# Optimization experiments

Hardware: AMD Instinct MI355X
Metric: run time of the kernel (lower is better)

Reference implementation:

```python
import jax, jax.numpy as jnp
import numpy as np

B, HD, NQ, NC, NH, NL, NP, NLAY, DFF = 8, 256, 300, 80, 8, 3, 4, 6, 1024
SHAPES = [(80, 80), (40, 40), (20, 20)]
FEAT_CH = [512, 1024, 2048]
DH = HD // NH
EPS_ANCHOR = 0.01


def _linear(x, w, b):
    return x @ w.T + b


def _ln(x, g, b):
    m = x.mean(-1, keepdims=True)
    v = ((x - m) ** 2).mean(-1, keepdims=True)
    return (x - m) / jnp.sqrt(v + 1e-5) * g + b


def _mlp3(x, w1, b1, w2, b2, w3, b3):
    x = jax.nn.relu(_linear(x, w1, b1))
    x = jax.nn.relu(_linear(x, w2, b2))
    return _linear(x, w3, b3)


def _inv_sigmoid(x, eps=1e-5):
    x = jnp.clip(x, 0.0, 1.0)
    return jnp.log(jnp.clip(x, eps, None) / jnp.clip(1.0 - x, eps, None))


def _anchors():
    parts = []
    for lvl, (h, w) in enumerate(SHAPES):
        gy, gx = jnp.meshgrid(jnp.arange(h, dtype=jnp.float32), jnp.arange(w, dtype=jnp.float32), indexing='ij')
        xy = jnp.stack([(gx + 0.5) / w, (gy + 0.5) / h], -1).reshape(-1, 2)
        wh = jnp.full_like(xy, 0.05 * (2.0 ** lvl))
        parts.append(jnp.concatenate([xy, wh], -1))
    a = jnp.concatenate(parts, 0)[None]  # [1, L, 4]
    valid = jnp.all((a > EPS_ANCHOR) & (a < 1 - EPS_ANCHOR), -1, keepdims=True)
    a = jnp.log(a / (1 - a))
    a = jnp.where(valid, a, jnp.float32(1e6))  # finite sentinel for torch's inf
    return a, valid.astype(jnp.float32)


def _mha(q_in, k_in, v_in, wqkv, bqkv, wo, bo):
    wq, wk, wv = jnp.split(wqkv, 3, 0)
    bq, bk, bv = jnp.split(bqkv, 3, 0)
    q = _linear(q_in, wq, bq)
    k = _linear(k_in, wk, bk)
    v = _linear(v_in, wv, bv)
    Bq = q.shape[0]
    sp = lambda t: t.reshape(Bq, -1, NH, DH).transpose(0, 2, 1, 3)
    q, k, v = sp(q), sp(k), sp(v)
    att = jax.nn.softmax(jnp.einsum('bhqd,bhkd->bhqk', q, k) * (1.0 / np.sqrt(DH)), -1)
    out = jnp.einsum('bhqk,bhkd->bhqd', att, v).transpose(0, 2, 1, 3).reshape(Bq, -1, HD)
    return _linear(out, wo, bo)


def _msda(value, loc, aw):
    # value [B,Len,NH,DH], loc [B,Q,NH,NL,NP,2] in [0,1], aw [B,Q,NH,NL,NP]
    Bq, Q = loc.shape[0], loc.shape[1]
    out = jnp.zeros((Bq, Q, NH, DH), value.dtype)
    start = 0
    for lvl, (h, w) in enumerate(SHAPES):
        v = value[:, start:start + h * w]  # [B,hw,NH,DH]
        start += h * w
        # grid_sample align_corners=False pixel coords
        x = loc[..., lvl, :, 0] * w - 0.5  # [B,Q,NH,NP]
        y = loc[..., lvl, :, 1] * h - 0.5
        x0 = jnp.floor(x)
        y0 = jnp.floor(y)
        lx = x - x0
        ly = y - y0
        acc = jnp.zeros((Bq, Q, NH, NP, DH), value.dtype)
        for dy, dx, wt in ((0, 0, (1 - lx) * (1 - ly)), (0, 1, lx * (1 - ly)), (1, 0, (1 - lx) * ly), (1, 1, lx * ly)):
            xi = x0 + dx
            yi = y0 + dy
            ok = ((xi >= 0) & (xi < w) & (yi >= 0) & (yi < h)).astype(value.dtype)  # zero padding
            idx = (jnp.clip(yi, 0, h - 1) * w + jnp.clip(xi, 0, w - 1)).astype(jnp.int32)
            idxf = idx.transpose(0, 1, 3, 2).reshape(Bq, Q * NP, NH)
            g = jnp.take_along_axis(v, idxf[..., None], axis=1)  # [B,Q*NP,NH,DH]
            g = g.reshape(Bq, Q, NP, NH, DH).transpose(0, 1, 3, 2, 4)
            acc = acc + g * (wt * ok)[..., None]
        out = out + (acc * aw[..., lvl, :, None]).sum(3)
    return out.reshape(Bq, Q, HD)


def reference(feat0, feat1, feat2, pw0, bg0, bb0, pw1, bg1, bb1, pw2, bg2, bb2,
              eo_w, eo_b, eln_g, eln_b, es_w, es_b,
              eb_w1, eb_b1, eb_w2, eb_b2, eb_w3, eb_b3,
              qp_w1, qp_b1, qp_w2, qp_b2,
              d_qkv_w, d_qkv_b, d_ao_w, d_ao_b, d_ln1_g, d_ln1_b,
              d_off_w, d_off_b, d_aw_w, d_aw_b, d_val_w, d_val_b,
              d_out_w, d_out_b, d_ln2_g, d_ln2_b,
              d_f1_w, d_f1_b, d_f2_w, d_f2_b, d_ln3_g, d_ln3_b,
              d_sc_w, d_sc_b, d_bb_w1, d_bb_b1, d_bb_w2, d_bb_b2, d_bb_w3, d_bb_b3):
    feats = [feat0, feat1, feat2]
    pws, bgs, bbs = [pw0, pw1, pw2], [bg0, bg1, bg2], [bb0, bb1, bb2]
    toks = []
    for f, pw, g, b in zip(feats, pws, bgs, bbs):
        # 1x1 conv (no bias) + BatchNorm eval (running mean 0, var 1 -> affine)
        t = jnp.einsum('bchw,oc->bhwo', f, pw) * g + b
        toks.append(t.reshape(f.shape[0], -1, HD))
    memory = jnp.concatenate(toks, 1)  # [B, 8400, 256]
    anchors, valid = _anchors()
    memory = memory * valid
    out_mem = _ln(_linear(memory, eo_w, eo_b), eln_g, eln_b)
    scores = _linear(out_mem, es_w, es_b)  # [B,L,NC]
    _, topi = jax.lax.top_k(scores.max(-1), NQ)  # 'default' query select
    gather = lambda t: jnp.take_along_axis(t, topi[..., None], axis=1)
    sel_mem = gather(out_mem)
    anc_b = jnp.broadcast_to(anchors, (memory.shape[0],) + anchors.shape[1:])
    ref_unact = _mlp3(sel_mem, eb_w1, eb_b1, eb_w2, eb_b2, eb_w3, eb_b3) + gather(anc_b)
    tgt = jax.lax.stop_gradient(sel_mem)
    ref = jax.nn.sigmoid(jax.lax.stop_gradient(ref_unact))  # [B,NQ,4]
    Bq = memory.shape[0]
    for i in range(NLAY):
        qpos = _linear(jax.nn.relu(_linear(ref, qp_w1, qp_b1)), qp_w2, qp_b2)
        q = tgt + qpos
        a = _mha(q, q, tgt, d_qkv_w[i], d_qkv_b[i], d_ao_w[i], d_ao_b[i])
        tgt = _ln(tgt + a, d_ln1_g[i], d_ln1_b[i])
        qc = tgt + qpos
        off = _linear(qc, d_off_w[i], d_off_b[i]).reshape(Bq, NQ, NH, NL, NP, 2)
        aw = jax.nn.softmax(_linear(qc, d_aw_w[i], d_aw_b[i]).reshape(Bq, NQ, NH, NL * NP), -1)
        aw = aw.reshape(Bq, NQ, NH, NL, NP)
        r = ref[:, :, None, None, None, :]
        loc = r[..., :2] + off / NP * r[..., 2:] * 0.5
        val = _linear(memory, d_val_w[i], d_val_b[i]).reshape(Bq, -1, NH, DH)
        ca = _linear(_msda(val, loc, aw), d_out_w[i], d_out_b[i])
        tgt = _ln(tgt + ca, d_ln2_g[i], d_ln2_b[i])
        f = _linear(jax.nn.relu(_linear(tgt, d_f1_w[i], d_f1_b[i])), d_f2_w[i], d_f2_b[i])
        tgt = _ln(tgt + f, d_ln3_g[i], d_ln3_b[i])
        delta = _mlp3(tgt, d_bb_w1[i], d_bb_b1[i], d_bb_w2[i], d_bb_b2[i], d_bb_w3[i], d_bb_b3[i])
        new_ref = jax.nn.sigmoid(delta + _inv_sigmoid(ref))
        ref = jax.lax.stop_gradient(new_ref) if i < NLAY - 1 else new_ref
    logits = _linear(tgt, d_sc_w[-1], d_sc_b[-1])
    return jnp.concatenate([logits, ref], -1)  # [B, NQ, NC+4]


def setup_inputs():
    key = jax.random.key(0)
    ks = iter(jax.random.split(key, 80))
    def rn(shape, s=0.02):
        return jax.random.normal(next(ks), shape, jnp.float32) * s
    inp = {}
    for i, (c, (h, w)) in enumerate(zip(FEAT_CH, SHAPES)):
        inp['feat%d' % i] = rn((B, c, h, w), 1.0)
        inp['pw%d' % i] = rn((HD, c), (2.0 / c) ** 0.5)
        inp['bg%d' % i] = jnp.ones((HD,), jnp.float32)
        inp['bb%d' % i] = jnp.zeros((HD,), jnp.float32)
    inp['eo_w'] = rn((HD, HD)); inp['eo_b'] = jnp.zeros((HD,), jnp.float32)
    inp['eln_g'] = jnp.ones((HD,), jnp.float32); inp['eln_b'] = jnp.zeros((HD,), jnp.float32)
    inp['es_w'] = rn((NC, HD)); inp['es_b'] = jnp.zeros((NC,), jnp.float32)
    inp['eb_w1'] = rn((HD, HD)); inp['eb_b1'] = jnp.zeros((HD,), jnp.float32)
    inp['eb_w2'] = rn((HD, HD)); inp['eb_b2'] = jnp.zeros((HD,), jnp.float32)
    inp['eb_w3'] = rn((4, HD)); inp['eb_b3'] = jnp.zeros((4,), jnp.float32)
    inp['qp_w1'] = rn((2 * HD, 4)); inp['qp_b1'] = jnp.zeros((2 * HD,), jnp.float32)
    inp['qp_w2'] = rn((HD, 2 * HD)); inp['qp_b2'] = jnp.zeros((HD,), jnp.float32)
    L = NLAY
    inp['d_qkv_w'] = rn((L, 3 * HD, HD)); inp['d_qkv_b'] = jnp.zeros((L, 3 * HD), jnp.float32)
    inp['d_ao_w'] = rn((L, HD, HD)); inp['d_ao_b'] = jnp.zeros((L, HD), jnp.float32)
    inp['d_ln1_g'] = jnp.ones((L, HD), jnp.float32); inp['d_ln1_b'] = jnp.zeros((L, HD), jnp.float32)
    inp['d_off_w'] = rn((L, NH * NL * NP * 2, HD), 0.005); inp['d_off_b'] = rn((L, NH * NL * NP * 2), 0.1)
    inp['d_aw_w'] = rn((L, NH * NL * NP, HD)); inp['d_aw_b'] = jnp.zeros((L, NH * NL * NP), jnp.float32)
    inp['d_val_w'] = rn((L, HD, HD)); inp['d_val_b'] = jnp.zeros((L, HD), jnp.float32)
    inp['d_out_w'] = rn((L, HD, HD)); inp['d_out_b'] = jnp.zeros((L, HD), jnp.float32)
    inp['d_ln2_g'] = jnp.ones((L, HD), jnp.float32); inp['d_ln2_b'] = jnp.zeros((L, HD), jnp.float32)
    inp['d_f1_w'] = rn((L, DFF, HD)); inp['d_f1_b'] = jnp.zeros((L, DFF), jnp.float32)
    inp['d_f2_w'] = rn((L, HD, DFF)); inp['d_f2_b'] = jnp.zeros((L, HD), jnp.float32)
    inp['d_ln3_g'] = jnp.ones((L, HD), jnp.float32); inp['d_ln3_b'] = jnp.zeros((L, HD), jnp.float32)
    inp['d_sc_w'] = rn((L, NC, HD)); inp['d_sc_b'] = jnp.zeros((L, NC), jnp.float32)
    inp['d_bb_w1'] = rn((L, HD, HD)); inp['d_bb_b1'] = jnp.zeros((L, HD), jnp.float32)
    inp['d_bb_w2'] = rn((L, HD, HD)); inp['d_bb_b2'] = jnp.zeros((L, HD), jnp.float32)
    inp['d_bb_w3'] = rn((L, 4, HD)); inp['d_bb_b3'] = jnp.zeros((L, 4), jnp.float32)
    return inp
```

## Files before the change

### kernel.cpp

```cpp
#include <hip/hip_runtime.h>

constexpr int Bb  = 8;
constexpr int HDn = 256;
constexpr int NQn = 300;
constexpr int NCn = 80;
constexpr int NHn = 8;
constexpr int NPn = 4;
constexpr int Sn  = 8400;
constexpr int MQ  = Bb * NQn;
constexpr int MS  = Bb * Sn;

typedef __attribute__((ext_vector_type(8))) short short8;
typedef __attribute__((ext_vector_type(4))) float floatx4;

__device__ __forceinline__ unsigned short f2bf(float f) {
    unsigned u = __float_as_uint(f);
    unsigned r = u + 0x7FFFu + ((u >> 16) & 1u);
    return (unsigned short)(r >> 16);
}
__device__ __forceinline__ unsigned pack2(float a, float b) {
    return (unsigned)f2bf(a) | ((unsigned)f2bf(b) << 16);
}

__global__ __launch_bounds__(256) void proj_kernel(
    const float* __restrict__ feat, const float* __restrict__ pw,
    const float* __restrict__ bg, const float* __restrict__ bb,
    float* __restrict__ mem,
    int C, int HW, int Wdim, int base)
{
    const int b = blockIdx.z;
    const float* Afeat = feat + (size_t)b * C * HW;
    __shared__ float As[16][128];
    __shared__ float Ws[16][128];
    const int tid = threadIdx.x;
    const int tx = tid & 15, ty = tid >> 4;
    const int p0 = blockIdx.y * 128, o0 = blockIdx.x * 128;
    const int pp4 = (tid & 31) * 4;
    const int cb = tid >> 5;
    const int wrow = tid >> 1, wk = (tid & 1) * 8;
    float acc[8][8] = {};
    for (int k0 = 0; k0 < C; k0 += 16) {
        float4 va0 = make_float4(0.f, 0.f, 0.f, 0.f), va1 = va0;
        if (p0 + pp4 < HW) {
            va0 = *reinterpret_cast<const float4*>(Afeat + (size_t)(k0 + cb) * HW + p0 + pp4);
            va1 = *reinterpret_cast<const float4*>(Afeat + (size_t)(k0 + cb + 8) * HW + p0 + pp4);
        }
        const float4 w0 = *reinterpret_cast<const float4*>(pw + (size_t)(o0 + wrow) * C + k0 + wk);
        const float4 w1 = *reinterpret_cast<const float4*>(pw + (size_t)(o0 + wrow) * C + k0 + wk + 4);
        __syncthreads();
        As[cb][pp4 + 0] = va0.x; As[cb][pp4 + 1] = va0.y; As[cb][pp4 + 2] = va0.z; As[cb][pp4 + 3] = va0.w;
        As[cb + 8][pp4 + 0] = va1.x; As[cb + 8][pp4 + 1] = va1.y; As[cb + 8][pp4 + 2] = va1.z; As[cb + 8][pp4 + 3] = va1.w;
        Ws[wk + 0][wrow] = w0.x; Ws[wk + 1][wrow] = w0.y; Ws[wk + 2][wrow] = w0.z; Ws[wk + 3][wrow] = w0.w;
        Ws[wk + 4][wrow] = w1.x; Ws[wk + 5][wrow] = w1.y; Ws[wk + 6][wrow] = w1.z; Ws[wk + 7][wrow] = w1.w;
        __syncthreads();
#pragma unroll
        for (int k = 0; k < 16; ++k) {
            const float4 a0 = *reinterpret_cast<const float4*>(&As[k][ty * 8]);
            const float4 a1 = *reinterpret_cast<const float4*>(&As[k][ty * 8 + 4]);
            const float4 wv0 = *reinterpret_cast<const float4*>(&Ws[k][tx * 8]);
            const float4 wv1 = *reinterpret_cast<const float4*>(&Ws[k][tx * 8 + 4]);
            const float av[8] = {a0.x, a0.y, a0.z, a0.w, a1.x, a1.y, a1.z, a1.w};
            const float wv[8] = {wv0.x, wv0.y, wv0.z, wv0.w, wv1.x, wv1.y, wv1.z, wv1.w};
#pragma unroll
            for (int i = 0; i < 8; ++i)
#pragma unroll
                for (int j = 0; j < 8; ++j)
                    acc[i][j] = fmaf(av[i], wv[j], acc[i][j]);
        }
    }
    float bgv[8], bbv[8];
#pragma unroll
    for (int j = 0; j < 8; ++j) { bgv[j] = bg[o0 + tx * 8 + j]; bbv[j] = bb[o0 + tx * 8 + j]; }
#pragma unroll
    for (int i = 0; i < 8; ++i) {
        const int pp = p0 + ty * 8 + i;
        if (pp >= HW) continue;
        const int yy = pp / Wdim, xx = pp - yy * Wdim;
        const float ax = (xx + 0.5f) / Wdim, ay = (yy + 0.5f) / Wdim;
        const float vm = ((ax > 0.01f) && (ax < 0.99f) && (ay > 0.01f) && (ay < 0.99f)) ? 1.f : 0.f;
        float* op = mem + ((size_t)b * Sn + base + pp) * HDn + o0;
#pragma unroll
        for (int j = 0; j < 8; ++j)
            op[tx * 8 + j] = (acc[i][j] * bgv[j] + bbv[j]) * vm;
    }
}

__global__ __launch_bounds__(512) void gemm_eoln(
    const float* __restrict__ A,
    const float* __restrict__ W,
    const float* __restrict__ bias,
    const float* __restrict__ g, const float* __restrict__ bt,
    float* __restrict__ O)
{
    __shared__ float As[16][128];
    __shared__ float Ws[16][256];
    const int tid = threadIdx.x;
    const int tx = tid & 31;
    const int ty = tid >> 5;
    const int m0 = blockIdx.x * 128;
    const int arow = tid >> 2, ak = (tid & 3) * 4;
    const int wrow = tid >> 1, wk = (tid & 1) * 8;
    float acc[8][8] = {};
    for (int k0 = 0; k0 < 256; k0 += 16) {
        const float4 a4 = *reinterpret_cast<const float4*>(A + (size_t)(m0 + arow) * 256 + k0 + ak);
        const float4 w0 = *reinterpret_cast<const float4*>(W + (size_t)wrow * 256 + k0 + wk);
        const float4 w1 = *reinterpret_cast<const float4*>(W + (size_t)wrow * 256 + k0 + wk + 4);
        __syncthreads();
        As[ak + 0][arow] = a4.x; As[ak + 1][arow] = a4.y; As[ak + 2][arow] = a4.z; As[ak + 3][arow] = a4.w;
        Ws[wk + 0][wrow] = w0.x; Ws[wk + 1][wrow] = w0.y; Ws[wk + 2][wrow] = w0.z; Ws[wk + 3][wrow] = w0.w;
        Ws[wk + 4][wrow] = w1.x; Ws[wk + 5][wrow] = w1.y; Ws[wk + 6][wrow] = w1.z; Ws[wk + 7][wrow] = w1.w;
        __syncthreads();
#pragma unroll
        for (int k = 0; k < 16; ++k) {
            const float4 a0 = *reinterpret_cast<const float4*>(&As[k][ty * 8]);
            const float4 a1 = *reinterpret_cast<const float4*>(&As[k][ty * 8 + 4]);
            const float4 wv0 = *reinterpret_cast<const float4*>(&Ws[k][tx * 8]);
            const float4 wv1 = *reinterpret_cast<const float4*>(&Ws[k][tx * 8 + 4]);
            const float av[8] = {a0.x, a0.y, a0.z, a0.w, a1.x, a1.y, a1.z, a1.w};
            const float wv[8] = {wv0.x, wv0.y, wv0.z, wv0.w, wv1.x, wv1.y, wv1.z, wv1.w};
#pragma unroll
            for (int i = 0; i < 8; ++i)
#pragma unroll
                for (int j = 0; j < 8; ++j)
                    acc[i][j] = fmaf(av[i], wv[j], acc[i][j]);
        }
    }
    float bv[8], gv[8], btv[8];
#pragma unroll
    for (int j = 0; j < 8; ++j) {
        bv[j] = bias[tx * 8 + j];
        gv[j] = g[tx * 8 + j];
        btv[j] = bt[tx * 8 + j];
    }
#pragma unroll
    for (int i = 0; i < 8; ++i) {
        float s1 = 0.f, s2 = 0.f;
#pragma unroll
        for (int j = 0; j < 8; ++j) {
            const float v = acc[i][j] + bv[j];
            acc[i][j] = v;
            s1 += v; s2 += v * v;
        }
#pragma unroll
        for (int o = 1; o < 32; o <<= 1) {
            s1 += __shfl_xor(s1, o, 64);
            s2 += __shfl_xor(s2, o, 64);
        }
        const float mean = s1 * (1.f / 256.f);
        const float var  = s2 * (1.f / 256.f) - mean * mean;
        const float inv  = rsqrtf(var + 1e-5f);
        float out[8];
#pragma unroll
        for (int j = 0; j < 8; ++j) out[j] = (acc[i][j] - mean) * inv * gv[j] + btv[j];
        float* op = O + (size_t)(m0 + ty * 8 + i) * 256 + tx * 8;
        *reinterpret_cast<float4*>(op) = make_float4(out[0], out[1], out[2], out[3]);
        *reinterpret_cast<float4*>(op + 4) = make_float4(out[4], out[5], out[6], out[7]);
    }
}

__global__ __launch_bounds__(256) void gemm_es(
    const float* __restrict__ A,
    const float* __restrict__ W,
    const float* __restrict__ bias,
    float* __restrict__ smax)
{
    __shared__ float As[16][128];
    __shared__ float Ws[16][80];
    const int tid = threadIdx.x;
    const int tx = tid & 15;
    const int ty = tid >> 4;
    const int m0 = blockIdx.x * 128;
    const int arow = tid >> 1, ak = (tid & 1) * 8;
    float acc[8][5] = {};
    for (int k0 = 0; k0 < 256; k0 += 16) {
        const float4 a0 = *reinterpret_cast<const float4*>(A + (size_t)(m0 + arow) * 256 + k0 + ak);
        const float4 a1 = *reinterpret_cast<const float4*>(A + (size_t)(m0 + arow) * 256 + k0 + ak + 4);
        float4 w0 = make_float4(0.f,0.f,0.f,0.f), w1 = w0;
        const int wrow = tid >> 1, wk = (tid & 1) * 8;
        if (tid < 160) {
            w0 = *reinterpret_cast<const float4*>(W + (size_t)wrow * 256 + k0 + wk);
            w1 = *reinterpret_cast<const float4*>(W + (size_t)wrow * 256 + k0 + wk + 4);
        }
        __syncthreads();
        As[ak + 0][arow] = a0.x; As[ak + 1][arow] = a0.y; As[ak + 2][arow] = a0.z; As[ak + 3][arow] = a0.w;
        As[ak + 4][arow] = a1.x; As[ak + 5][arow] = a1.y; As[ak + 6][arow] = a1.z; As[ak + 7][arow] = a1.w;
        if (tid < 160) {
            Ws[wk + 0][wrow] = w0.x; Ws[wk + 1][wrow] = w0.y; Ws[wk + 2][wrow] = w0.z; Ws[wk + 3][wrow] = w0.w;
            Ws[wk + 4][wrow] = w1.x; Ws[wk + 5][wrow] = w1.y; Ws[wk + 6][wrow] = w1.z; Ws[wk + 7][wrow] = w1.w;
        }
        __syncthreads();
#pragma unroll
        for (int k = 0; k < 16; ++k) {
            const float4 a4 = *reinterpret_cast<const float4*>(&As[k][ty * 8]);
            const float4 a5 = *reinterpret_cast<const float4*>(&As[k][ty * 8 + 4]);
            const float av[8] = {a4.x, a4.y, a4.z, a4.w, a5.x, a5.y, a5.z, a5.w};
            float wv[5];
#pragma unroll
            for (int j = 0; j < 5; ++j) wv[j] = Ws[k][tx * 5 + j];
#pragma unroll
            for (int i = 0; i < 8; ++i)
#pragma unroll
                for (int j = 0; j < 5; ++j)
                    acc[i][j] = fmaf(av[i], wv[j], acc[i][j]);
        }
    }
    float bv[5];
#pragma unroll
    for (int j = 0; j < 5; ++j) bv[j] = bias[tx * 5 + j];
#pragma unroll
    for (int i = 0; i < 8; ++i) {
        float vmax = -3.0e38f;
#pragma unroll
        for (int j = 0; j < 5; ++j) vmax = fmaxf(vmax, acc[i][j] + bv[j]);
#pragma unroll
        for (int o = 1; o < 16; o <<= 1) vmax = fmaxf(vmax, __shfl_xor(vmax, o, 64));
        if (tx == 0) smax[m0 + ty * 8 + i] = vmax;
    }
}

__global__ void fconv_kernel(const float* __restrict__ in, unsigned short* __restrict__ out, int n4)
{
    const int i = blockIdx.x * 256 + threadIdx.x;
    if (i >= n4) return;
    const float4 v = reinterpret_cast<const float4*>(in)[i];
    reinterpret_cast<uint2*>(out)[i] = make_uint2(pack2(v.x, v.y), pack2(v.z, v.w));
}

__global__ __launch_bounds__(512) void gemm_vbig(
    const unsigned short* __restrict__ A,
    const float* __restrict__ W,
    const float* __restrict__ bias,
    unsigned short* __restrict__ C, int ldc,
    int M)
{
    __shared__ __align__(16) unsigned short As[128 * 40];
    __shared__ __align__(16) unsigned short Bs[256 * 40];
    const int tid = threadIdx.x;
    const int lane = tid & 63, wid = tid >> 6;
    const int wm = wid >> 2, wn = wid & 3;
    const int m0 = blockIdx.x * 128, n0 = blockIdx.y * 256;
    const int arow = tid >> 2, ak = (tid & 3) * 8;
    const int brow = tid >> 1, bk = (tid & 1) * 16;
    const int fs = (lane >> 4) * 8;
    floatx4 acc[4][4];
#pragma unroll
    for (int i = 0; i < 4; ++i)
#pragma unroll
        for (int j = 0; j < 4; ++j) acc[i][j] = (floatx4){0.f, 0.f, 0.f, 0.f};

    for (int k0 = 0; k0 < 256; k0 += 32) {
        const short8 a8 = *reinterpret_cast<const short8*>(A + (size_t)(m0 + arow) * 256 + k0 + ak);
        float wv[16];
        {
            const float* wp = W + (size_t)(n0 + brow) * 256 + k0 + bk;
#pragma unroll
            for (int j = 0; j < 4; ++j) *reinterpret_cast<float4*>(&wv[4 * j]) = *reinterpret_cast<const float4*>(wp + 4 * j);
        }
        __syncthreads();
        *reinterpret_cast<short8*>(&As[arow * 40 + ak]) = a8;
        *reinterpret_cast<uint4*>(&Bs[brow * 40 + bk]) =
            make_uint4(pack2(wv[0], wv[1]), pack2(wv[2], wv[3]), pack2(wv[4], wv[5]), pack2(wv[6], wv[7]));
        *reinterpret_cast<uint4*>(&Bs[brow * 40 + bk + 8]) =
            make_uint4(pack2(wv[8], wv[9]), pack2(wv[10], wv[11]), pack2(wv[12], wv[13]), pack2(wv[14], wv[15]));
        __syncthreads();
        short8 af[4], bf[4];
#pragma unroll
        for (int mi = 0; mi < 4; ++mi)
            af[mi] = *reinterpret_cast<const short8*>(&As[(wm * 64 + mi * 16 + (lane & 15)) * 40 + fs]);
#pragma unroll
        for (int ni = 0; ni < 4; ++ni)
            bf[ni] = *reinterpret_cast<const short8*>(&Bs[(wn * 64 + ni * 16 + (lane & 15)) * 40 + fs]);
#pragma unroll
        for (int mi = 0; mi < 4; ++mi)
#pragma unroll
            for (int ni = 0; ni < 4; ++ni)
                acc[mi][ni] = __builtin_amdgcn_mfma_f32_16x16x32_bf16(af[mi], bf[ni], acc[mi][ni], 0, 0, 0);
    }
#pragma unroll
    for (int mi = 0; mi < 4; ++mi) {
        const int rowb = m0 + wm * 64 + mi * 16 + (lane >> 4) * 4;
#pragma unroll
        for (int ni = 0; ni < 4; ++ni) {
            const int col = n0 + wn * 64 + ni * 16 + (lane & 15);
            const float bv = bias[col];
#pragma unroll
            for (int r = 0; r < 4; ++r)
                C[(size_t)(rowb + r) * ldc + col] = f2bf(acc[mi][ni][r] + bv);
        }
    }
}

template <int ACT>
__global__ __launch_bounds__(256) void gemm_sm(
    const float* __restrict__ A, const float* __restrict__ A2, int a2_nlim, int lda,
    const float* __restrict__ W, int ldw,
    const float* __restrict__ bias,
    float* __restrict__ C, int ldc,
    int M, int N, int K)
{
    constexpr int LD = 264;
    __shared__ __align__(16) unsigned short As[64 * LD];
    __shared__ __align__(16) unsigned short Bs[64 * LD];
    const int tid = threadIdx.x;
    const int lane = tid & 63, wid = tid >> 6;
    const int wr = wid >> 1, wc = wid & 1;
    const int m0 = blockIdx.y * 64, n0 = blockIdx.x * 64;
    const float* A2e = (A2 && n0 < a2_nlim) ? A2 : nullptr;
    const int srow = tid >> 2;
    const int cb   = (tid & 3) * 16;
    const int fs = (lane >> 4) * 8;
    floatx4 acc[2][2];
#pragma unroll
    for (int i = 0; i < 2; ++i)
#pragma unroll
        for (int j = 0; j < 2; ++j) acc[i][j] = (floatx4){0.f, 0.f, 0.f, 0.f};

    for (int kc = 0; kc < K; kc += 256) {
        if (kc) __syncthreads();
        {
            const bool mok = (m0 + srow < M);
            const float* ap = A + (size_t)(m0 + srow) * lda + kc;
            const float* ap2 = A2e ? A2e + (size_t)(m0 + srow) * lda + kc : nullptr;
#pragma unroll
            for (int c = 0; c < 4; ++c) {
                float4 v[4];
#pragma unroll
                for (int j = 0; j < 4; ++j) {
                    v[j] = make_float4(0.f, 0.f, 0.f, 0.f);
                    if (mok) {
                        v[j] = *reinterpret_cast<const float4*>(ap + cb + c * 64 + j * 4);
                        if (ap2) {
                            const float4 v2 = *reinterpret_cast<const float4*>(ap2 + cb + c * 64 + j * 4);
                            v[j].x += v2.x; v[j].y += v2.y; v[j].z += v2.z; v[j].w += v2.w;
                        }
                    }
                }
#pragma unroll
                for (int j = 0; j < 4; ++j)
                    *reinterpret_cast<uint2*>(&As[srow * LD + cb + c * 64 + j * 4]) =
                        make_uint2(pack2(v[j].x, v[j].y), pack2(v[j].z, v[j].w));
            }
        }
        {
            const bool nok = (n0 + srow < N);
            const float* wp = W + (size_t)(n0 + srow) * ldw + kc;
#pragma unroll
            for (int c = 0; c < 4; ++c) {
                float4 v[4];
#pragma unroll
                for (int j = 0; j < 4; ++j) {
                    v[j] = make_float4(0.f, 0.f, 0.f, 0.f);
                    if (nok) v[j] = *reinterpret_cast<const float4*>(wp + cb + c * 64 + j * 4);
                }
#pragma unroll
                for (int j = 0; j < 4; ++j)
                    *reinterpret_cast<uint2*>(&Bs[srow * LD + cb + c * 64 + j * 4]) =
                        make_uint2(pack2(v[j].x, v[j].y), pack2(v[j].z, v[j].w));
            }
        }
        __syncthreads();
#pragma unroll
        for (int ks = 0; ks < 8; ++ks) {
            short8 af[2], bf[2];
#pragma unroll
            for (int mi = 0; mi < 2; ++mi)
                af[mi] = *reinterpret_cast<const short8*>(&As[(wr * 32 + mi * 16 + (lane & 15)) * LD + ks * 32 + fs]);
#pragma unroll
            for (int ni = 0; ni < 2; ++ni)
                bf[ni] = *reinterpret_cast<const short8*>(&Bs[(wc * 32 + ni * 16 + (lane & 15)) * LD + ks * 32 + fs]);
#pragma unroll
            for (int mi = 0; mi < 2; ++mi)
#pragma unroll
                for (int ni = 0; ni < 2; ++ni)
                    acc[mi][ni] = __builtin_amdgcn_mfma_f32_16x16x32_bf16(af[mi], bf[ni], acc[mi][ni], 0, 0, 0);
        }
    }
#pragma unroll
    for (int mi = 0; mi < 2; ++mi) {
        const int rowb = m0 + wr * 32 + mi * 16 + (lane >> 4) * 4;
#pragma unroll
        for (int ni = 0; ni < 2; ++ni) {
            const int col = n0 + wc * 32 + ni * 16 + (lane & 15);
            if (col >= N) continue;
            const float bv = bias[col];
#pragma unroll
            for (int r = 0; r < 4; ++r) {
                const int row = rowb + r;
                if (row >= M) continue;
                float v = acc[mi][ni][r] + bv;
                if (ACT == 1) v = fmaxf(v, 0.f);
                C[(size_t)row * ldc + col] = v;
            }
        }
    }
}

__global__ __launch_bounds__(256) void gemm_qpos(
    const float* __restrict__ ref, const float* __restrict__ w1, const float* __restrict__ b1,
    const float* __restrict__ W2, const float* __restrict__ b2,
    float* __restrict__ C, int M)
{
    __shared__ __align__(16) unsigned short As_h[128 * 40];
    __shared__ __align__(16) unsigned short Bs_h[128 * 40];
    __shared__ float w1s[512 * 4];
    __shared__ float b1s[512];
    const int tid = threadIdx.x;
    const int lane = tid & 63, wid = tid >> 6;
    const int wm = wid >> 1, wn = wid & 1;
    const int m0 = blockIdx.x * 128, n0 = blockIdx.y * 128;
    const int srow = tid >> 1, skoff = (tid & 1) * 16;
    const int fs = (lane >> 4) * 8;
    for (int i = tid; i < 512 * 4; i += 256) w1s[i] = w1[i];
    for (int i = tid; i < 512; i += 256) b1s[i] = b1[i];
    float rv0 = 0.f, rv1 = 0.f, rv2 = 0.f, rv3 = 0.f;
    if (m0 + srow < M) {
        const float* rp = ref + (size_t)(m0 + srow) * 4;
        rv0 = rp[0]; rv1 = rp[1]; rv2 = rp[2]; rv3 = rp[3];
    }
    floatx4 acc[4][4];
#pragma unroll
    for (int i = 0; i < 4; ++i)
#pragma unroll
        for (int j = 0; j < 4; ++j) acc[i][j] = (floatx4){0.f, 0.f, 0.f, 0.f};
    __syncthreads();

    for (int k0 = 0; k0 < 512; k0 += 32) {
        float av[16], wv[16];
#pragma unroll
        for (int j = 0; j < 16; ++j) {
            const int k = k0 + skoff + j;
            const float v = b1s[k] + rv0 * w1s[k * 4] + rv1 * w1s[k * 4 + 1] + rv2 * w1s[k * 4 + 2] + rv3 * w1s[k * 4 + 3];
            av[j] = fmaxf(v, 0.f);
            wv[j] = 0.f;
        }
        if (n0 + srow < 256) {
            const float* wp = W2 + (size_t)(n0 + srow) * 512 + k0 + skoff;
#pragma unroll
            for (int j = 0; j < 4; ++j) *reinterpret_cast<float4*>(&wv[4 * j]) = *reinterpret_cast<const float4*>(wp + 4 * j);
        }
        __syncthreads();
        *reinterpret_cast<uint4*>(&As_h[srow * 40 + skoff]) =
            make_uint4(pack2(av[0], av[1]), pack2(av[2], av[3]), pack2(av[4], av[5]), pack2(av[6], av[7]));
        *reinterpret_cast<uint4*>(&As_h[srow * 40 + skoff + 8]) =
            make_uint4(pack2(av[8], av[9]), pack2(av[10], av[11]), pack2(av[12], av[13]), pack2(av[14], av[15]));
        *reinterpret_cast<uint4*>(&Bs_h[srow * 40 + skoff]) =
            make_uint4(pack2(wv[0], wv[1]), pack2(wv[2], wv[3]), pack2(wv[4], wv[5]), pack2(wv[6], wv[7]));
        *reinterpret_cast<uint4*>(&Bs_h[srow * 40 + skoff + 8]) =
            make_uint4(pack2(wv[8], wv[9]), pack2(wv[10], wv[11]), pack2(wv[12], wv[13]), pack2(wv[14], wv[15]));
        __syncthreads();
        short8 af[4], bff[4];
#pragma unroll
        for (int mi = 0; mi < 4; ++mi) {
            const int r = wm * 64 + mi * 16 + (lane & 15);
            af[mi] = *reinterpret_cast<const short8*>(&As_h[r * 40 + fs]);
        }
#pragma unroll
        for (int ni = 0; ni < 4; ++ni) {
            const int r = wn * 64 + ni * 16 + (lane & 15);
            bff[ni] = *reinterpret_cast<const short8*>(&Bs_h[r * 40 + fs]);
        }
#pragma unroll
        for (int mi = 0; mi < 4; ++mi)
#pragma unroll
            for (int ni = 0; ni < 4; ++ni)
                acc[mi][ni] = __builtin_amdgcn_mfma_f32_16x16x32_bf16(af[mi], bff[ni], acc[mi][ni], 0, 0, 0);
    }
#pragma unroll
    for (int mi = 0; mi < 4; ++mi) {
        const int rowb = m0 + wm * 64 + mi * 16 + (lane >> 4) * 4;
#pragma unroll
        for (int ni = 0; ni < 4; ++ni) {
            const int col = n0 + wn * 64 + ni * 16 + (lane & 15);
            const float bv = b2[col];
#pragma unroll
            for (int r = 0; r < 4; ++r) {
                const int row = rowb + r;
                if (row >= M) continue;
                C[(size_t)row * HDn + col] = acc[mi][ni][r] + bv;
            }
        }
    }
}

__global__ __launch_bounds__(256) void ln_kernel(
    const float* __restrict__ X, const float* __restrict__ R,
    const float* __restrict__ g, const float* __restrict__ bta,
    float* __restrict__ O)
{
    const int m = blockIdx.x;
    const int t = threadIdx.x;
    float v = X[(size_t)m * HDn + t] + R[(size_t)m * HDn + t];
    float s1 = v, s2 = v * v;
#pragma unroll
    for (int o = 32; o > 0; o >>= 1) {
        s1 += __shfl_down(s1, o, 64);
        s2 += __shfl_down(s2, o, 64);
    }
    __shared__ float a1[4], a2[4];
    if ((t & 63) == 0) { a1[t >> 6] = s1; a2[t >> 6] = s2; }
    __syncthreads();
    const float S1 = a1[0] + a1[1] + a1[2] + a1[3];
    const float S2 = a2[0] + a2[1] + a2[2] + a2[3];
    const float mean = S1 * (1.f / HDn);
    const float var  = S2 * (1.f / HDn) - mean * mean;
    const float inv  = rsqrtf(var + 1e-5f);
    O[(size_t)m * HDn + t] = (v - mean) * inv * g[t] + bta[t];
}

__global__ __launch_bounds__(256) void topk_kernel(const float* __restrict__ smax, int* __restrict__ topi)
{
    const int b = blockIdx.x, t = threadIdx.x;
    __shared__ float vals[Sn];
    __shared__ int hist[256];
    __shared__ unsigned long long sel[NQn];
    __shared__ unsigned long long s_prefix;
    __shared__ int s_need;
    __shared__ int s_cnt;
    for (int i = t; i < Sn; i += 256) vals[i] = smax[(size_t)b * Sn + i];
    if (t == 0) { s_prefix = 0ULL; s_need = NQn; s_cnt = 0; }
    __syncthreads();

    for (int shift = 56; shift >= 0; shift -= 8) {
        if (t < 256) hist[t] = 0;
        __syncthreads();
        const unsigned long long prefix = s_prefix;
        const unsigned long long mask = (shift == 56) ? 0ULL : (~0ULL << (shift + 8));
        for (int i = t; i < Sn; i += 256) {
            unsigned uk = __float_as_uint(vals[i]);
            uk = (uk & 0x80000000u) ? ~uk : (uk | 0x80000000u);
            const unsigned long long key = ((unsigned long long)uk << 32) | (unsigned)(Sn - i);
            if ((key & mask) == prefix)
                atomicAdd(&hist[(int)((key >> shift) & 255)], 1);
        }
        __syncthreads();
        if (t == 0) {
            int need = s_need, accum = 0, v = 255;
            for (; v >= 0; --v) {
                const int c = hist[v];
                if (accum + c >= need) break;
                accum += c;
            }
            s_prefix = s_prefix | ((unsigned long long)(unsigned)v << shift);
            s_need = need - accum;
        }
        __syncthreads();
    }
    const unsigned long long thresh = s_prefix;
    for (int i = t; i < Sn; i += 256) {
        unsigned uk = __float_as_uint(vals[i]);
        uk = (uk & 0x80000000u) ? ~uk : (uk | 0x80000000u);
        const unsigned long long key = ((unsigned long long)uk << 32) | (unsigned)(Sn - i);
        if (key >= thresh) {
            const int pos = atomicAdd(&s_cnt, 1);
            if (pos < NQn) sel[pos] = key;
        }
    }
    __syncthreads();
    for (int j = t; j < NQn; j += 256) {
        const unsigned long long kj = sel[j];
        int rank = 0;
        for (int i = 0; i < NQn; ++i) rank += (sel[i] > kj) ? 1 : 0;
        topi[b * NQn + rank] = Sn - (int)(kj & 0xFFFFFFFFULL);
    }
}

__global__ __launch_bounds__(256) void gather_kernel(const float* __restrict__ src, const int* __restrict__ topi,
                                                     float* __restrict__ dst)
{
    const int m = blockIdx.x;
    const int b = m / NQn;
    const int s = topi[m];
    dst[(size_t)m * HDn + threadIdx.x] = src[((size_t)b * Sn + s) * HDn + threadIdx.x];
}

__device__ __forceinline__ void anchor_of(int s, float a[4])
{
    int lvl, p, w;
    if (s < 6400)      { lvl = 0; p = s;        w = 80; }
    else if (s < 8000) { lvl = 1; p = s - 6400; w = 40; }
    else               { lvl = 2; p = s - 8000; w = 20; }
    const int y = p / w, x = p - y * w;
    const float ax = (x + 0.5f) / w, ay = (y + 0.5f) / w;
    const float awh = 0.05f * (float)(1 << lvl);
    const bool valid = (ax > 0.01f) && (ax < 0.99f) && (ay > 0.01f) && (ay < 0.99f);
    if (valid) {
        a[0] = logf(ax / (1.f - ax));
        a[1] = logf(ay / (1.f - ay));
        const float lw = logf(awh / (1.f - awh));
        a[2] = lw; a[3] = lw;
    } else {
        a[0] = a[1] = a[2] = a[3] = 1e6f;
    }
}

template <int MODE>
__global__ __launch_bounds__(256) void head4_kernel(
    const float* __restrict__ A, const float* __restrict__ W, const float* __restrict__ bias,
    const int* __restrict__ topi, float* __restrict__ ref)
{
    const int wv = threadIdx.x >> 6, lane = threadIdx.x & 63;
    const int m = blockIdx.x * 4 + wv;
    if (m >= MQ) return;
    const float4 a = *reinterpret_cast<const float4*>(A + (size_t)m * HDn + lane * 4);
    float d[4];
#pragma unroll
    for (int c = 0; c < 4; ++c) {
        const float4 w = *reinterpret_cast<const float4*>(W + c * HDn + lane * 4);
        float p = a.x * w.x + a.y * w.y + a.z * w.z + a.w * w.w;
#pragma unroll
        for (int o = 32; o > 0; o >>= 1) p += __shfl_xor(p, o, 64);
        d[c] = p;
    }
    if (lane == 0) {
        float base[4];
        if (MODE == 0) {
            anchor_of(topi[m], base);
        } else {
#pragma unroll
            for (int c = 0; c < 4; ++c) {
                float x = ref[m * 4 + c];
                x = fminf(fmaxf(x, 0.f), 1.f);
                base[c] = logf(fmaxf(x, 1e-5f) / fmaxf(1.f - x, 1e-5f));
            }
        }
#pragma unroll
        for (int c = 0; c < 4; ++c) {
            const float x = d[c] + bias[c] + base[c];
            ref[m * 4 + c] = 1.f / (1.f + expf(-x));
        }
    }
}

__global__ __launch_bounds__(320) void mha_kernel(const float* __restrict__ QKV, float* __restrict__ O)
{
    const int h = blockIdx.x, b = blockIdx.y, qs = blockIdx.z;
    __shared__ float Ks[NQn][32];
    __shared__ float Vs[NQn][32];
    __shared__ float Om[152][32];
    __shared__ float Mm[152];
    __shared__ float Lm[152];
    const int t = threadIdx.x;
    for (int i = t; i < NQn * 32; i += 320) {
        const int kk = i >> 5, d = i & 31;
        const size_t src = ((size_t)(b * NQn + kk)) * 768 + h * 32 + d;
        Ks[kk][d] = QKV[src + 256];
        Vs[kk][d] = QKV[src + 512];
    }
    __syncthreads();
    const int half = (t >= 160) ? 1 : 0;
    const int qloc = half ? (t - 160) : t;
    const int q = qs * 150 + qloc;
    float m = -1e30f, l = 0.f;
    float o[32];
    if (qloc < 150) {
        float qv[32];
        const float* qp = QKV + ((size_t)(b * NQn + q)) * 768 + h * 32;
#pragma unroll
        for (int d = 0; d < 32; ++d) qv[d] = qp[d] * 0.17677669529663687f;
#pragma unroll
        for (int d = 0; d < 32; ++d) o[d] = 0.f;
        const int k0 = half * 150, k1 = k0 + 150;
        for (int kk = k0; kk < k1; ++kk) {
            float s0 = 0.f, s1 = 0.f, s2 = 0.f, s3 = 0.f;
#pragma unroll
            for (int d = 0; d < 32; d += 4) {
                s0 = fmaf(qv[d + 0], Ks[kk][d + 0], s0);
                s1 = fmaf(qv[d + 1], Ks[kk][d + 1], s1);
                s2 = fmaf(qv[d + 2], Ks[kk][d + 2], s2);
                s3 = fmaf(qv[d + 3], Ks[kk][d + 3], s3);
            }
            const float s = (s0 + s1) + (s2 + s3);
            if (s > m + 8.f) {
                const float cf = __expf(m - s);
                m = s;
                l *= cf;
#pragma unroll
                for (int d = 0; d < 32; ++d) o[d] *= cf;
            }
            const float pv = __expf(s - m);
            l += pv;
#pragma unroll
            for (int d = 0; d < 32; ++d) o[d] = fmaf(pv, Vs[kk][d], o[d]);
        }
        if (half) {
            Mm[qloc] = m; Lm[qloc] = l;
#pragma unroll
            for (int d = 0; d < 32; ++d) Om[qloc][d] = o[d];
        }
    }
    __syncthreads();
    if (!half && qloc < 150) {
        const float m2 = Mm[qloc], l2 = Lm[qloc];
        const float mm = fmaxf(m, m2);
        const float c1 = __expf(m - mm), c2 = __expf(m2 - mm);
        const float L = l * c1 + l2 * c2;
        const float inv = 1.f / L;
        float* op = O + ((size_t)(b * NQn + q)) * HDn + h * 32;
#pragma unroll
        for (int d = 0; d < 32; ++d) op[d] = (o[d] * c1 + Om[qloc][d] * c2) * inv;
    }
}

__global__ void concat_oaw(const float* __restrict__ offw, const float* __restrict__ offbias,
                           const float* __restrict__ aww, const float* __restrict__ awbias,
                           float* __restrict__ cw, float* __restrict__ cb)
{
    const int idx = blockIdx.x * 256 + threadIdx.x;
    const int TW = 6 * 288 * 256;
    if (idx < TW) {
        const int i = idx / (288 * 256);
        const int r = (idx / 256) % 288;
        const int c = idx & 255;
        cw[idx] = (r < 192) ? offw[((size_t)i * 192 + r) * 256 + c]
                            : aww[((size_t)i * 96 + (r - 192)) * 256 + c];
    } else if (idx < TW + 6 * 288) {
        const int j = idx - TW;
        const int i = j / 288, r = j % 288;
        cb[j] = (r < 192) ? offbias[i * 192 + r] : awbias[i * 96 + (r - 192)];
    }
}

__global__ __launch_bounds__(256) void msda_kernel(const unsigned short* __restrict__ val, int ldv,
                                                   const float* __restrict__ oaw,
                                                   const float* __restrict__ ref,
                                                   float* __restrict__ out)
{
    const int mq = blockIdx.x;
    const int b = mq / NQn;
    const int t = threadIdx.x;
    const int h = t >> 5, d = t & 31;
    __shared__ float s_ref[4];
    __shared__ float s_aw[96];
    __shared__ float s_off[192];
    if (t < 4) s_ref[t] = ref[mq * 4 + t];
    if (t < 96) s_aw[t] = oaw[(size_t)mq * 288 + 192 + t];
    if (t < 192) s_off[t] = oaw[(size_t)mq * 288 + t];
    __syncthreads();
    if (t < 8) {
        float* p = s_aw + t * 12;
        float mx = -1e30f;
#pragma unroll
        for (int i = 0; i < 12; ++i) mx = fmaxf(mx, p[i]);
        float e[12];
        float s = 0.f;
#pragma unroll
        for (int i = 0; i < 12; ++i) { e[i] = expf(p[i] - mx); s += e[i]; }
        const float inv = 1.f / s;
#pragma unroll
        for (int i = 0; i < 12; ++i) p[i] = e[i] * inv;
    }
    __syncthreads();
    const int Wl[3] = {80, 40, 20};
    const int base[3] = {0, 6400, 8000};
    float acc = 0.f;
#pragma unroll
    for (int l = 0; l < 3; ++l) {
        const int W = Wl[l];
        const unsigned short* vb = val + ((size_t)b * Sn + base[l]) * ldv + h * 32 + d;
#pragma unroll
        for (int p = 0; p < 4; ++p) {
            const float ox = s_off[((h * 3 + l) * 4 + p) * 2 + 0];
            const float oy = s_off[((h * 3 + l) * 4 + p) * 2 + 1];
            const float locx = s_ref[0] + ox * (1.f / NPn) * s_ref[2] * 0.5f;
            const float locy = s_ref[1] + oy * (1.f / NPn) * s_ref[3] * 0.5f;
            const float x = locx * W - 0.5f;
            const float y = locy * W - 0.5f;
            const float x0f = floorf(x), y0f = floorf(y);
            const float lx = x - x0f, ly = y - y0f;
            const int x0 = (int)x0f, y0 = (int)y0f;
            const float a = s_aw[h * 12 + l * 4 + p];
            const float wts[4] = {(1.f - lx) * (1.f - ly), lx * (1.f - ly), (1.f - lx) * ly, lx * ly};
            float sum = 0.f;
#pragma unroll
            for (int c2 = 0; c2 < 4; ++c2) {
                const int xi = x0 + (c2 & 1);
                const int yi = y0 + (c2 >> 1);
                const bool ok = (xi >= 0) && (xi < W) && (yi >= 0) && (yi < W);
                const int xc = min(max(xi, 0), W - 1);
                const int yc = min(max(yi, 0), W - 1);
                const float v = __uint_as_float((unsigned)vb[(size_t)(yc * W + xc) * ldv] << 16);
                sum = fmaf(wts[c2], ok ? v : 0.f, sum);
            }
            acc = fmaf(a, sum, acc);
        }
    }
    out[(size_t)mq * HDn + t] = acc;
}

__global__ void copy_ref_kernel(const float* __restrict__ ref, float* __restrict__ out)
{
    const int m = blockIdx.x * 256 + threadIdx.x;
    if (m >= MQ) return;
#pragma unroll
    for (int c = 0; c < 4; ++c) out[(size_t)m * 84 + 80 + c] = ref[m * 4 + c];
}

extern "C" void kernel_launch(void* const* d_in, const int* in_sizes, int n_in,
                              void* d_out, int out_size, void* d_ws, size_t ws_size,
                              hipStream_t stream)
{
    (void)in_sizes; (void)n_in; (void)out_size;
    const float* feat0 = (const float*)d_in[0];
    const float* pw0   = (const float*)d_in[1];
    const float* bg0   = (const float*)d_in[2];
    const float* bb0   = (const float*)d_in[3];
    const float* feat1 = (const float*)d_in[4];
    const float* pw1   = (const float*)d_in[5];
    const float* bg1   = (const float*)d_in[6];
    const float* bb1   = (const float*)d_in[7];
    const float* feat2 = (const float*)d_in[8];
    const float* pw2   = (const float*)d_in[9];
    const float* bg2   = (const float*)d_in[10];
    const float* bb2   = (const float*)d_in[11];
    const float* eo_w  = (const float*)d_in[12];
    const float* eo_b  = (const float*)d_in[13];
    const float* eln_g = (const float*)d_in[14];
    const float* eln_b = (const float*)d_in[15];
    const float* es_w  = (const float*)d_in[16];
    const float* es_b  = (const float*)d_in[17];
    const float* eb_w1 = (const float*)d_in[18];
    const float* eb_b1 = (const float*)d_in[19];
    const float* eb_w2 = (const float*)d_in[20];
    const float* eb_b2 = (const float*)d_in[21];
    const float* eb_w3 = (const float*)d_in[22];
    const float* eb_b3 = (const float*)d_in[23];
    const float* qp_w1 = (const float*)d_in[24];
    const float* qp_b1 = (const float*)d_in[25];
    const float* qp_w2 = (const float*)d_in[26];
    const float* qp_b2 = (const float*)d_in[27];
    const float* d_qkv_w = (const float*)d_in[28];
    const float* d_qkv_b = (const float*)d_in[29];
    const float* d_ao_w  = (const float*)d_in[30];
    const float* d_ao_b  = (const float*)d_in[31];
    const float* d_ln1_g = (const float*)d_in[32];
    const float* d_ln1_b = (const float*)d_in[33];
    const float* d_off_w = (const float*)d_in[34];
    const float* d_off_b = (const float*)d_in[35];
    const float* d_aw_w  = (const float*)d_in[36];
    const float* d_aw_b  = (const float*)d_in[37];
    const float* d_val_w = (const float*)d_in[38];
    const float* d_val_b = (const float*)d_in[39];
    const float* d_out_w = (const float*)d_in[40];
    const float* d_out_b = (const float*)d_in[41];
    const float* d_ln2_g = (const float*)d_in[42];
    const float* d_ln2_b = (const float*)d_in[43];
    const float* d_f1_w  = (const float*)d_in[44];
    const float* d_f1_b  = (const float*)d_in[45];
    const float* d_f2_w  = (const float*)d_in[46];
    const float* d_f2_b  = (const float*)d_in[47];
    const float* d_ln3_g = (const float*)d_in[48];
    const float* d_ln3_b = (const float*)d_in[49];
    const float* d_sc_w  = (const float*)d_in[50];
    const float* d_sc_b  = (const float*)d_in[51];
    const float* d_bb_w1 = (const float*)d_in[52];
    const float* d_bb_b1 = (const float*)d_in[53];
    const float* d_bb_w2 = (const float*)d_in[54];
    const float* d_bb_b2 = (const float*)d_in[55];
    const float* d_bb_w3 = (const float*)d_in[56];
    const float* d_bb_b3 = (const float*)d_in[57];

    float* ws = (float*)d_ws;
    size_t off = 0;
    auto alloc = [&](size_t n) { float* p = ws + off; off += (n + 63) & ~(size_t)63; return p; };
    float* memory = alloc((size_t)MS * HDn);
    float* om     = alloc((size_t)MS * HDn);
    float* smaxb  = alloc((size_t)MS);
    int*   topi   = (int*)alloc((size_t)MQ);
    float* tgt    = alloc((size_t)MQ * HDn);
    float* refb   = alloc((size_t)MQ * 4);
    float* qpos   = alloc((size_t)MQ * HDn);
    float* qkvb   = alloc((size_t)MQ * 768);
    float* atto   = alloc((size_t)MQ * HDn);
    float* abuf   = alloc((size_t)MQ * HDn);
    float* oawb   = alloc((size_t)MQ * 288);
    float* msd    = alloc((size_t)MQ * HDn);
    float* ffb    = alloc((size_t)MQ * 1024);
    float* qb     = alloc((size_t)MQ * HDn);
    float* kb     = alloc((size_t)MQ * HDn);
    float* cw     = alloc((size_t)6 * 288 * 256);
    float* cb     = alloc((size_t)6 * 288);
    const size_t VALBIG_FLOATS = (size_t)MS * 768;
    unsigned short* valbig = nullptr;
    if ((off + VALBIG_FLOATS + 64) * sizeof(float) <= ws_size)
        valbig = (unsigned short*)alloc(VALBIG_FLOATS);
    const bool batched = (valbig != nullptr);
    unsigned short* ombf = (unsigned short*)om;
    float* outp = (float*)d_out;

    concat_oaw<<<(6 * 288 * 256 + 6 * 288 + 255) / 256, 256, 0, stream>>>(d_off_w, d_off_b, d_aw_w, d_aw_b, cw, cb);

    proj_kernel<<<dim3(2, 50, 8), 256, 0, stream>>>(feat0, pw0, bg0, bb0, memory, 512, 6400, 80, 0);
    proj_kernel<<<dim3(2, 13, 8), 256, 0, stream>>>(feat1, pw1, bg1, bb1, memory, 1024, 1600, 40, 6400);
    proj_kernel<<<dim3(2, 4, 8), 256, 0, stream>>>(feat2, pw2, bg2, bb2, memory, 2048, 400, 20, 8000);

    gemm_eoln<<<525, 512, 0, stream>>>(memory, eo_w, eo_b, eln_g, eln_b, om);
    gemm_es<<<525, 256, 0, stream>>>(om, es_w, es_b, smaxb);
    topk_kernel<<<Bb, 256, 0, stream>>>(smaxb, topi);
    gather_kernel<<<MQ, 256, 0, stream>>>(om, topi, tgt);

    gemm_sm<1><<<dim3(4, 38), 256, 0, stream>>>(tgt, nullptr, 0, HDn, eb_w1, HDn, eb_b1, qb, HDn, MQ, HDn, HDn);
    gemm_sm<1><<<dim3(4, 38), 256, 0, stream>>>(qb, nullptr, 0, HDn, eb_w2, HDn, eb_b2, kb, HDn, MQ, HDn, HDn);
    head4_kernel<0><<<600, 256, 0, stream>>>(kb, eb_w3, eb_b3, topi, refb);

    if (batched) {
        fconv_kernel<<<(MS * HDn / 4 + 255) / 256, 256, 0, stream>>>(memory, ombf, MS * HDn / 4);
        gemm_vbig<<<dim3(525, 6), 512, 0, stream>>>(ombf, d_val_w, d_val_b, valbig, 1536, MS);
    }

    for (int i = 0; i < 6; ++i) {
        const float* wqkv = d_qkv_w + (size_t)i * 768 * 256;
        const float* bqkv = d_qkv_b + (size_t)i * 768;
        gemm_qpos<<<dim3(19, 2), 256, 0, stream>>>(refb, qp_w1, qp_b1, qp_w2, qp_b2, qpos, MQ);
        gemm_sm<0><<<dim3(12, 38), 256, 0, stream>>>(tgt, qpos, 512, HDn, wqkv, HDn, bqkv, qkvb, 768, MQ, 768, HDn);
        mha_kernel<<<dim3(NHn, Bb, 2), 320, 0, stream>>>(qkvb, atto);
        gemm_sm<0><<<dim3(4, 38), 256, 0, stream>>>(atto, nullptr, 0, HDn, d_ao_w + (size_t)i * 65536, HDn,
                                                    d_ao_b + (size_t)i * 256, abuf, HDn, MQ, HDn, HDn);
        ln_kernel<<<MQ, 256, 0, stream>>>(abuf, tgt, d_ln1_g + (size_t)i * 256, d_ln1_b + (size_t)i * 256, tgt);
        gemm_sm<0><<<dim3(5, 38), 256, 0, stream>>>(tgt, qpos, 1 << 30, HDn, cw + (size_t)i * 288 * 256, HDn,
                                                    cb + (size_t)i * 288, oawb, 288, MQ, 288, HDn);
        const unsigned short* valptr;
        int ldv;
        if (batched) { valptr = valbig + (size_t)i * 256; ldv = 1536; }
        else {
            fconv_kernel<<<(MS * HDn / 4 + 255) / 256, 256, 0, stream>>>(memory, (unsigned short*)ffb, MS * HDn / 4);
            gemm_vbig<<<dim3(525, 1), 512, 0, stream>>>((unsigned short*)ffb, d_val_w + (size_t)i * 65536,
                                                        d_val_b + (size_t)i * 256, ombf, 256, MS);
            valptr = ombf; ldv = 256;
        }
        msda_kernel<<<MQ, 256, 0, stream>>>(valptr, ldv, oawb, refb, msd);
        gemm_sm<0><<<dim3(4, 38), 256, 0, stream>>>(msd, nullptr, 0, HDn, d_out_w + (size_t)i * 65536, HDn,
                                                    d_out_b + (size_t)i * 256, abuf, HDn, MQ, HDn, HDn);
        ln_kernel<<<MQ, 256, 0, stream>>>(abuf, tgt, d_ln2_g + (size_t)i * 256, d_ln2_b + (size_t)i * 256, tgt);
        gemm_sm<1><<<dim3(16, 38), 256, 0, stream>>>(tgt, nullptr, 0, HDn, d_f1_w + (size_t)i * 1024 * 256, HDn,
                                                     d_f1_b + (size_t)i * 1024, ffb, 1024, MQ, 1024, HDn);
        gemm_sm<0><<<dim3(4, 38), 256, 0, stream>>>(ffb, nullptr, 0, 1024, d_f2_w + (size_t)i * 256 * 1024, 1024,
                                                    d_f2_b + (size_t)i * 256, abuf, HDn, MQ, HDn, 1024);
        ln_kernel<<<MQ, 256, 0, stream>>>(abuf, tgt, d_ln3_g + (size_t)i * 256, d_ln3_b + (size_t)i * 256, tgt);
        gemm_sm<1><<<dim3(4, 38), 256, 0, stream>>>(tgt, nullptr, 0, HDn, d_bb_w1 + (size_t)i * 65536, HDn,
                                                    d_bb_b1 + (size_t)i * 256, qb, HDn, MQ, HDn, HDn);
        gemm_sm<1><<<dim3(4, 38), 256, 0, stream>>>(qb, nullptr, 0, HDn, d_bb_w2 + (size_t)i * 65536, HDn,
                                                    d_bb_b2 + (size_t)i * 256, kb, HDn, MQ, HDn, HDn);
        head4_kernel<1><<<600, 256, 0, stream>>>(kb, d_bb_w3 + (size_t)i * 1024, d_bb_b3 + (size_t)i * 4, nullptr, refb);
    }

    gemm_sm<0><<<dim3(2, 38), 256, 0, stream>>>(tgt, nullptr, 0, HDn, d_sc_w + (size_t)5 * 80 * 256, HDn,
                                                d_sc_b + (size_t)5 * 80, outp, 84, MQ, NCn, HDn);
    copy_ref_kernel<<<(MQ + 255) / 256, 256, 0, stream>>>(refb, outp);
}
```

Measured before the change: 2.543 ms.

## Fuse bf16 memory conversion and ref copy; restripe proj_kernel column mapping

gemm_eoln now writes a bf16 copy of memory while it loads its A tiles, which replaces the separate fconv_kernel pass over the full memory tensor. head4_kernel writes the final reference boxes straight into the output on the last layer, so copy_ref_kernel is gone. proj_kernel switches to a strided column mapping (tx + 16*j) with a scalar LDS read per column instead of float4 reads, and its launch bounds gain a min-blocks hint of 2. These changes remove one memory-sized pass and one launch, but they need extra workspace for the bf16 buffer and may raise register pressure in proj_kernel.

New measurement: 2.662 ms. 4.7% more time.

```diff
diff --git a/kernel.cpp b/kernel.cpp
--- a/kernel.cpp
+++ b/kernel.cpp
@@ -22,7 +22,7 @@
     return (unsigned)f2bf(a) | ((unsigned)f2bf(b) << 16);
 }
 
-__global__ __launch_bounds__(256) void proj_kernel(
+__global__ __launch_bounds__(256, 2) void proj_kernel(
     const float* __restrict__ feat, const float* __restrict__ pw,
     const float* __restrict__ bg, const float* __restrict__ bb,
     float* __restrict__ mem,
@@ -57,10 +57,10 @@
         for (int k = 0; k < 16; ++k) {
             const float4 a0 = *reinterpret_cast<const float4*>(&As[k][ty * 8]);
             const float4 a1 = *reinterpret_cast<const float4*>(&As[k][ty * 8 + 4]);
-            const float4 wv0 = *reinterpret_cast<const float4*>(&Ws[k][tx * 8]);
-            const float4 wv1 = *reinterpret_cast<const float4*>(&Ws[k][tx * 8 + 4]);
             const float av[8] = {a0.x, a0.y, a0.z, a0.w, a1.x, a1.y, a1.z, a1.w};
-            const float wv[8] = {wv0.x, wv0.y, wv0.z, wv0.w, wv1.x, wv1.y, wv1.z, wv1.w};
+            float wv[8];
+#pragma unroll
+            for (int j = 0; j < 8; ++j) wv[j] = Ws[k][tx + 16 * j];
 #pragma unroll
             for (int i = 0; i < 8; ++i)
 #pragma unroll
@@ -70,7 +70,7 @@
     }
     float bgv[8], bbv[8];
 #pragma unroll
-    for (int j = 0; j < 8; ++j) { bgv[j] = bg[o0 + tx * 8 + j]; bbv[j] = bb[o0 + tx * 8 + j]; }
+    for (int j = 0; j < 8; ++j) { bgv[j] = bg[o0 + tx + 16 * j]; bbv[j] = bb[o0 + tx + 16 * j]; }
 #pragma unroll
     for (int i = 0; i < 8; ++i) {
         const int pp = p0 + ty * 8 + i;
@@ -81,7 +81,7 @@
         float* op = mem + ((size_t)b * Sn + base + pp) * HDn + o0;
 #pragma unroll
         for (int j = 0; j < 8; ++j)
-            op[tx * 8 + j] = (acc[i][j] * bgv[j] + bbv[j]) * vm;
+            op[tx + 16 * j] = (acc[i][j] * bgv[j] + bbv[j]) * vm;
     }
 }
 
@@ -90,7 +90,8 @@
     const float* __restrict__ W,
     const float* __restrict__ bias,
     const float* __restrict__ g, const float* __restrict__ bt,
-    float* __restrict__ O)
+    float* __restrict__ O,
+    unsigned short* __restrict__ Abf)
 {
     __shared__ float As[16][128];
     __shared__ float Ws[16][256];
@@ -105,6 +106,9 @@
         const float4 a4 = *reinterpret_cast<const float4*>(A + (size_t)(m0 + arow) * 256 + k0 + ak);
         const float4 w0 = *reinterpret_cast<const float4*>(W + (size_t)wrow * 256 + k0 + wk);
         const float4 w1 = *reinterpret_cast<const float4*>(W + (size_t)wrow * 256 + k0 + wk + 4);
+        if (Abf)
+            *reinterpret_cast<uint2*>(Abf + (size_t)(m0 + arow) * 256 + k0 + ak) =
+                make_uint2(pack2(a4.x, a4.y), pack2(a4.z, a4.w));
         __syncthreads();
         As[ak + 0][arow] = a4.x; As[ak + 1][arow] = a4.y; As[ak + 2][arow] = a4.z; As[ak + 3][arow] = a4.w;
         Ws[wk + 0][wrow] = w0.x; Ws[wk + 1][wrow] = w0.y; Ws[wk + 2][wrow] = w0.z; Ws[wk + 3][wrow] = w0.w;
@@ -596,7 +600,7 @@
 template <int MODE>
 __global__ __launch_bounds__(256) void head4_kernel(
     const float* __restrict__ A, const float* __restrict__ W, const float* __restrict__ bias,
-    const int* __restrict__ topi, float* __restrict__ ref)
+    const int* __restrict__ topi, float* __restrict__ ref, float* __restrict__ outref)
 {
     const int wv = threadIdx.x >> 6, lane = threadIdx.x & 63;
     const int m = blockIdx.x * 4 + wv;
@@ -626,7 +630,9 @@
 #pragma unroll
         for (int c = 0; c < 4; ++c) {
             const float x = d[c] + bias[c] + base[c];
-            ref[m * 4 + c] = 1.f / (1.f + expf(-x));
+            const float r = 1.f / (1.f + expf(-x));
+            ref[m * 4 + c] = r;
+            if (outref) outref[(size_t)m * 84 + 80 + c] = r;
         }
     }
 }
@@ -785,14 +791,6 @@
         }
     }
     out[(size_t)mq * HDn + t] = acc;
-}
-
-__global__ void copy_ref_kernel(const float* __restrict__ ref, float* __restrict__ out)
-{
-    const int m = blockIdx.x * 256 + threadIdx.x;
-    if (m >= MQ) return;
-#pragma unroll
-    for (int c = 0; c < 4; ++c) out[(size_t)m * 84 + 80 + c] = ref[m * 4 + c];
 }
 
 extern "C" void kernel_launch(void* const* d_in, const int* in_sizes, int n_in,
@@ -880,9 +878,13 @@
     float* cw     = alloc((size_t)6 * 288 * 256);
     float* cb     = alloc((size_t)6 * 288);
     const size_t VALBIG_FLOATS = (size_t)MS * 768;
+    const size_t MEMBF_FLOATS  = (size_t)MS * 128;
     unsigned short* valbig = nullptr;
-    if ((off + VALBIG_FLOATS + 64) * sizeof(float) <= ws_size)
+    unsigned short* membf  = nullptr;
+    if ((off + VALBIG_FLOATS + MEMBF_FLOATS + 128) * sizeof(float) <= ws_size) {
         valbig = (unsigned short*)alloc(VALBIG_FLOATS);
+        membf  = (unsigned short*)alloc(MEMBF_FLOATS);
+    }
     const bool batched = (valbig != nullptr);
     unsigned short* ombf = (unsigned short*)om;
     float* outp = (float*)d_out;
@@ -893,19 +895,17 @@
     proj_kernel<<<dim3(2, 13, 8), 256, 0, stream>>>(feat1, pw1, bg1, bb1, memory, 1024, 1600, 40, 6400);
     proj_kernel<<<dim3(2, 4, 8), 256, 0, stream>>>(feat2, pw2, bg2, bb2, memory, 2048, 400, 20, 8000);
 
-    gemm_eoln<<<525, 512, 0, stream>>>(memory, eo_w, eo_b, eln_g, eln_b, om);
+    gemm_eoln<<<525, 512, 0, stream>>>(memory, eo_w, eo_b, eln_g, eln_b, om, batched ? membf : nullptr);
     gemm_es<<<525, 256, 0, stream>>>(om, es_w, es_b, smaxb);
     topk_kernel<<<Bb, 256, 0, stream>>>(smaxb, topi);
     gather_kernel<<<MQ, 256, 0, stream>>>(om, topi, tgt);
 
     gemm_sm<1><<<dim3(4, 38), 256, 0, stream>>>(tgt, nullptr, 0, HDn, eb_w1, HDn, eb_b1, qb, HDn, MQ, HDn, HDn);
     gemm_sm<1><<<dim3(4, 38), 256, 0, stream>>>(qb, nullptr, 0, HDn, eb_w2, HDn, eb_b2, kb, HDn, MQ, HDn, HDn);
-    head4_kernel<0><<<600, 256, 0, stream>>>(kb, eb_w3, eb_b3, topi, refb);
-
-    if (batched) {
-        fconv_kernel<<<(MS * HDn / 4 + 255) / 256, 256, 0, stream>>>(memory, ombf, MS * HDn / 4);
-        gemm_vbig<<<dim3(525, 6), 512, 0, stream>>>(ombf, d_val_w, d_val_b, valbig, 1536, MS);
-    }
+    head4_kernel<0><<<600, 256, 0, stream>>>(kb, eb_w3, eb_b3, topi, refb, nullptr);
+
+    if (batched)
+        gemm_vbig<<<dim3(525, 6), 512, 0, stream>>>(membf, d_val_w, d_val_b, valbig, 1536, MS);
 
     for (int i = 0; i < 6; ++i) {
         const float* wqkv = d_qkv_w + (size_t)i * 768 * 256;
@@ -940,10 +940,10 @@
                                                     d_bb_b1 + (size_t)i * 256, qb, HDn, MQ, HDn, HDn);
         gemm_sm<1><<<dim3(4, 38), 256, 0, stream>>>(qb, nullptr, 0, HDn, d_bb_w2 + (size_t)i * 65536, HDn,
                                                     d_bb_b2 + (size_t)i * 256, kb, HDn, MQ, HDn, HDn);
-        head4_kernel<1><<<600, 256, 0, stream>>>(kb, d_bb_w3 + (size_t)i * 1024, d_bb_b3 + (size_t)i * 4, nullptr, refb);
+        head4_kernel<1><<<600, 256, 0, stream>>>(kb, d_bb_w3 + (size_t)i * 1024, d_bb_b3 + (size_t)i * 4,
+                                                 nullptr, refb, (i == 5) ? outp : nullptr);
     }
 
     gemm_sm<0><<<dim3(2, 38), 256, 0, stream>>>(tgt, nullptr, 0, HDn, d_sc_w + (size_t)5 * 80 * 256, HDn,
                                                 d_sc_b + (size_t)5 * 80, outp, 84, MQ, NCn, HDn);
-    copy_ref_kernel<<<(MQ + 255) / 256, 256, 0, stream>>>(refb, outp);
-}
+}
```
